# Kernel optimization log

Measured on AMD Instinct MI355X. Metric: run time of the kernel, lower is better.

Reference implementation:

```python
import jax, jax.numpy as jnp
import numpy as np

H = 64
N_BENE, N_DIAG, N_TREAT = 200000, 10000, 100000
E = 1000000
N_INST = 500000

def setup_inputs() -> dict:
    key = jax.random.key(0)
    ks = jax.random.split(key, 24)
    def lin(k, din, dout):
        kw, kb = jax.random.split(k)
        s = 1.0 / np.sqrt(din)
        return (jax.random.uniform(kw, (din, dout), jnp.float32, -s, s),
                jax.random.uniform(kb, (dout,), jnp.float32, -s, s))
    inp = {
        'bene_ids': jax.random.randint(ks[0], (N_BENE,), 0, 10000, jnp.int32),
        'diag_ids': jax.random.randint(ks[1], (N_DIAG,), 0, 200, jnp.int32),
        'treatment_ids': jax.random.randint(ks[2], (N_TREAT,), 0, 1000, jnp.int32),
        'b2d_src': jax.random.randint(ks[3], (E,), 0, N_BENE, jnp.int32),
        'b2d_dst': jax.random.randint(ks[4], (E,), 0, N_DIAG, jnp.int32),
        't2d_src': jax.random.randint(ks[5], (E,), 0, N_TREAT, jnp.int32),
        't2d_dst': jax.random.randint(ks[6], (E,), 0, N_DIAG, jnp.int32),
        'inst2type': jax.random.randint(ks[7], (N_INST,), 0, N_DIAG, jnp.int32),
        'bene_emb': jax.random.normal(ks[8], (10000, H), jnp.float32),
        'diag_emb': jax.random.normal(ks[9], (200, H), jnp.float32),
        'treat_emb': jax.random.normal(ks[10], (1000, H), jnp.float32),
    }
    # two conv layers: msg_bene_to_diag (Wb,bb), msg_treatment_to_diag (Wt,bt), update_diag (Wu,bu)
    names = ['Wb0','bb0','Wt0','bt0','Wu0','bu0','Wb1','bb1','Wt1','bt1','Wu1','bu1']
    idx = 11
    for i in range(0, len(names), 2):
        W, b = lin(ks[idx], H, H); idx += 1
        inp[names[i]] = W; inp[names[i+1]] = b
    inp['oW1'], inp['ob1'] = lin(ks[idx], H, H // 2); idx += 1
    inp['oW2'], inp['ob2'] = lin(ks[idx], H // 2, 1)
    return inp

def _conv(bene, diag, treat, b2d_src, b2d_dst, t2d_src, t2d_dst, Wb, bb, Wt, bt, Wu, bu):
    msg_b = bene[b2d_src] @ Wb + bb                      # [E, H]
    agg_b = jax.ops.segment_sum(msg_b, b2d_dst, num_segments=N_DIAG)
    msg_t = treat[t2d_src] @ Wt + bt                     # [E, H]
    agg_t = jax.ops.segment_sum(msg_t, t2d_dst, num_segments=N_DIAG)
    combined = 0.5 * (agg_b + agg_t)                     # mean over 2 message types
    return combined @ Wu + bu

def reference(bene_ids, diag_ids, treatment_ids, b2d_src, b2d_dst, t2d_src, t2d_dst,
              inst2type, bene_emb, diag_emb, treat_emb,
              Wb0, bb0, Wt0, bt0, Wu0, bu0, Wb1, bb1, Wt1, bt1, Wu1, bu1,
              oW1, ob1, oW2, ob2):
    bene = bene_emb[bene_ids]
    diag = diag_emb[diag_ids]
    treat = treat_emb[treatment_ids]
    for (Wb, bb, Wt, bt, Wu, bu) in ((Wb0, bb0, Wt0, bt0, Wu0, bu0),
                                     (Wb1, bb1, Wt1, bt1, Wu1, bu1)):
        diag = _conv(bene, diag, treat, b2d_src, b2d_dst, t2d_src, t2d_dst,
                     Wb, bb, Wt, bt, Wu, bu)
        bene, diag, treat = jax.nn.relu(bene), jax.nn.relu(diag), jax.nn.relu(treat)
    inst = diag[inst2type]                               # [N_INST, H]
    h = jax.nn.relu(inst @ oW1 + ob1)                    # dropout is eval-mode identity
    return jax.nn.sigmoid(h @ oW2 + ob2)[:, 0]
```

## Files before the change

kernel.cpp:

```cpp
#include <hip/hip_runtime.h>
#include <hip/hip_bf16.h>

#define Hdim 64
#define NDIAG 10000
#define NEDGE 1000000
#define NINST 500000

#define NSUP 79
#define SSHIFT 7
#define SMASK 127
#define CAP_S 13568
#define BUFK 96
#define EPB 3907
#define NSPLIT 4
#define FPSCALE 1048576.0f
#define FPINV (1.0f / 1048576.0f)

__global__ __launch_bounds__(512) void split_kernel(
    const int* __restrict__ b2d_dst, const int* __restrict__ b2d_src, const int* __restrict__ bene_ids,
    const int* __restrict__ t2d_dst, const int* __restrict__ t2d_src, const int* __restrict__ treat_ids,
    int* __restrict__ gcur_b, int* __restrict__ gbuf_b,
    int* __restrict__ gcur_t, int* __restrict__ gbuf_t) {
    const int ty = blockIdx.y;
    const int* dst  = ty ? t2d_dst  : b2d_dst;
    const int* src  = ty ? t2d_src  : b2d_src;
    const int* ids  = ty ? treat_ids: bene_ids;
    int* gcur = ty ? gcur_t : gcur_b;
    int* gbuf = ty ? gbuf_t : gbuf_b;

    __shared__ int buf[NSUP][BUFK];
    __shared__ int cnt[NSUP];
    __shared__ int base_s[NSUP];
    const int tid = threadIdx.x;
    for (int i = tid; i < NSUP; i += 512) cnt[i] = 0;
    __syncthreads();

    const int base = blockIdx.x * EPB;
    const int end = min(NEDGE, base + EPB);
    for (int e = base + tid; e < end; e += 512) {
        int d = dst[e];
        int c = ids[src[e]];
        int b = d >> SSHIFT;
        int v = ((d & SMASK) << 16) | c;
        int p = atomicAdd(&cnt[b], 1);
        if (p < BUFK) {
            buf[b][p] = v;
        } else {
            int gp = atomicAdd(&gcur[b], 1);
            if (gp < CAP_S) gbuf[b * CAP_S + gp] = v;
        }
    }
    __syncthreads();

    const int wid = tid >> 6, lane = tid & 63;
    if (wid < 2) {
        int b = (wid << 6) + lane;
        if (b < NSUP) {
            int n = min(cnt[b], BUFK);
            base_s[b] = atomicAdd(&gcur[b], n);
        }
    }
    __syncthreads();

    for (int b = wid; b < NSUP; b += 8) {
        int n = min(cnt[b], BUFK);
        int gp0 = base_s[b];
        for (int k = lane; k < n; k += 64) {
            int gp = gp0 + k;
            if (gp < CAP_S) gbuf[b * CAP_S + gp] = buf[b][k];
        }
    }
}

__global__ __launch_bounds__(512) void agg_kernel(
    const int* __restrict__ gbuf_b, const int* __restrict__ gcur_b, const float* __restrict__ bene_emb,
    const int* __restrict__ gbuf_t, const int* __restrict__ gcur_t, const float* __restrict__ treat_emb,
    int* __restrict__ pbuf, int* __restrict__ pbufd) {
    const int bk = blockIdx.x, ty = blockIdx.y, sp = blockIdx.z;
    const int* gbuf  = ty ? gbuf_t : gbuf_b;
    const int* gcur  = ty ? gcur_t : gcur_b;
    const float* emb = ty ? treat_emb : bene_emb;

    __shared__ int acc[128][64];
    __shared__ int dcw[8][2][64];

    const int tid = threadIdx.x;
    const int wid = tid >> 6, lane = tid & 63;
    int4* a4 = (int4*)&acc[0][0];
    for (int i = tid; i < 2048; i += 512) a4[i] = int4{0, 0, 0, 0};
    __syncthreads();

    const int count = min(gcur[bk], CAP_S);
    const int slice = (count + NSPLIT - 1) / NSPLIT;
    const int s0 = sp * slice;
    const int s1 = min(count, s0 + slice);
    const int n = max(0, s1 - s0);
    const int nfull = n >> 6;
    const int rem = n & 63;
    const int* bucket = gbuf + bk * CAP_S;

    int dc0 = 0, dc1 = 0;
    for (int ck = wid; ck < nfull; ck += 8) {
        int vv = bucket[s0 + (ck << 6) + lane];
        #pragma unroll
        for (int g = 0; g < 8; ++g) {
            int dl[8]; float vf[8];
            #pragma unroll
            for (int u = 0; u < 8; ++u) {
                int s = __builtin_amdgcn_readlane(vv, g * 8 + u);
                dl[u] = (s >> 16) & SMASK;
                vf[u] = emb[(s & 0xffff) * Hdim + lane];
            }
            #pragma unroll
            for (int u = 0; u < 8; ++u) {
                atomicAdd(&acc[dl[u]][lane], (int)(fmaxf(vf[u], 0.f) * FPSCALE));
                dc0 += ((dl[u] < 64) & (lane == (dl[u] & 63))) ? 1 : 0;
                dc1 += ((dl[u] >= 64) & (lane == (dl[u] & 63))) ? 1 : 0;
            }
        }
    }
    if (rem && wid == (nfull & 7)) {
        int base2 = s0 + (nfull << 6);
        int vv = (lane < rem) ? bucket[base2 + lane] : 0;
        for (int u = 0; u < rem; ++u) {
            int s = __builtin_amdgcn_readlane(vv, u);
            int dl = (s >> 16) & SMASK;
            float vf = emb[(s & 0xffff) * Hdim + lane];
            atomicAdd(&acc[dl][lane], (int)(fmaxf(vf, 0.f) * FPSCALE));
            dc0 += ((dl < 64) & (lane == (dl & 63))) ? 1 : 0;
            dc1 += ((dl >= 64) & (lane == (dl & 63))) ? 1 : 0;
        }
    }
    dcw[wid][0][lane] = dc0;
    dcw[wid][1][lane] = dc1;
    __syncthreads();

    int4* o4 = (int4*)(pbuf + (size_t)((ty * NSUP + bk) * NSPLIT + sp) * 8192);
    for (int i = tid; i < 2048; i += 512) o4[i] = a4[i];
    if (tid < 128) {
        int t = 0;
        #pragma unroll
        for (int w = 0; w < 8; ++w) t += dcw[w][tid >> 6][tid & 63];
        pbufd[(size_t)((ty * NSUP + bk) * NSPLIT + sp) * 128 + tid] = t;
    }
}

__global__ __launch_bounds__(256) void head_kernel(
    const int* __restrict__ pbuf, const int* __restrict__ pbufd,
    const float* __restrict__ Wb1, const float* __restrict__ bb1,
    const float* __restrict__ Wt1, const float* __restrict__ bt1,
    const float* __restrict__ Wu1, const float* __restrict__ bu1,
    const float* __restrict__ oW1, const float* __restrict__ ob1,
    const float* __restrict__ oW2, const float* __restrict__ ob2,
    float* __restrict__ per_diag_out) {
    int wave = threadIdx.x >> 6;
    int lane = threadIdx.x & 63;
    int d = blockIdx.x * 4 + wave;

    __shared__ float Sb[4][64];
    __shared__ float St[4][64];
    __shared__ float Cc[4][64];
    __shared__ float Dd[4][64];

    const int bk = d >> SSHIFT, row = d & SMASK;
    const int* pb = pbuf + (size_t)(bk * NSPLIT) * 8192;
    const int* pt = pbuf + (size_t)((NSUP + bk) * NSPLIT) * 8192;
    int sbi = 0, sti = 0, dgb = 0, dgt = 0;
    #pragma unroll
    for (int sp = 0; sp < NSPLIT; ++sp) {
        sbi += pb[sp * 8192 + row * 64 + lane];
        sti += pt[sp * 8192 + row * 64 + lane];
        dgb += pbufd[(size_t)(bk * NSPLIT + sp) * 128 + row];
        dgt += pbufd[(size_t)((NSUP + bk) * NSPLIT + sp) * 128 + row];
    }
    Sb[wave][lane] = (float)sbi * FPINV;
    St[wave][lane] = (float)sti * FPINV;
    __syncthreads();

    float ab = (float)dgb * bb1[lane];
    float at = (float)dgt * bt1[lane];
    #pragma unroll 8
    for (int l = 0; l < Hdim; ++l) {
        ab += Sb[wave][l] * Wb1[l * Hdim + lane];
        at += St[wave][l] * Wt1[l * Hdim + lane];
    }
    float comb = 0.5f * (ab + at);
    Cc[wave][lane] = comb;
    __syncthreads();

    float dg = bu1[lane];
    #pragma unroll 8
    for (int l = 0; l < Hdim; ++l) dg += Cc[wave][l] * Wu1[l * Hdim + lane];
    float d1 = fmaxf(dg, 0.f);
    Dd[wave][lane] = d1;
    __syncthreads();

    float contrib = 0.f;
    if (lane < 32) {
        float h = ob1[lane];
        #pragma unroll 8
        for (int l = 0; l < Hdim; ++l) h += Dd[wave][l] * oW1[l * 32 + lane];
        h = fmaxf(h, 0.f);
        contrib = h * oW2[lane];
    }
    for (int o = 32; o > 0; o >>= 1) contrib += __shfl_down(contrib, o);
    if (lane == 0) {
        float logit = contrib + ob2[0];
        per_diag_out[d] = 1.f / (1.f + __expf(-logit));
    }
}

__global__ void gather_kernel(const int* __restrict__ inst2type,
                              const float* __restrict__ per_diag_out,
                              float* __restrict__ out) {
    int i = blockIdx.x * blockDim.x + threadIdx.x;
    int i4 = i * 4;
    if (i4 >= NINST) return;
    int4 t = *reinterpret_cast<const int4*>(inst2type + i4);
    float4 r;
    r.x = per_diag_out[t.x];
    r.y = per_diag_out[t.y];
    r.z = per_diag_out[t.z];
    r.w = per_diag_out[t.w];
    *reinterpret_cast<float4*>(out + i4) = r;
}

extern "C" void kernel_launch(void* const* d_in, const int* in_sizes, int n_in,
                              void* d_out, int out_size, void* d_ws, size_t ws_size,
                              hipStream_t stream) {
    (void)in_sizes; (void)n_in; (void)out_size; (void)ws_size;

    const int*   bene_ids  = (const int*)d_in[0];
    const int*   treat_ids = (const int*)d_in[2];
    const int*   b2d_src   = (const int*)d_in[3];
    const int*   b2d_dst   = (const int*)d_in[4];
    const int*   t2d_src   = (const int*)d_in[5];
    const int*   t2d_dst   = (const int*)d_in[6];
    const int*   inst2type = (const int*)d_in[7];
    const float* bene_emb  = (const float*)d_in[8];
    const float* treat_emb = (const float*)d_in[10];
    const float* Wb1 = (const float*)d_in[17];
    const float* bb1 = (const float*)d_in[18];
    const float* Wt1 = (const float*)d_in[19];
    const float* bt1 = (const float*)d_in[20];
    const float* Wu1 = (const float*)d_in[21];
    const float* bu1 = (const float*)d_in[22];
    const float* oW1 = (const float*)d_in[23];
    const float* ob1 = (const float*)d_in[24];
    const float* oW2 = (const float*)d_in[25];
    const float* ob2 = (const float*)d_in[26];
    float* out = (float*)d_out;

    char* w = (char*)d_ws;
    auto alloc = [&](size_t bytes) {
        char* p = w;
        w += (bytes + 255) & ~(size_t)255;
        return p;
    };
    int* gcur_all = (int*)alloc(2 * NSUP * 4);
    int* gcur_b = gcur_all;
    int* gcur_t = gcur_all + NSUP;
    int* gbuf_b = (int*)alloc((size_t)NSUP * CAP_S * 4);
    int* gbuf_t = (int*)alloc((size_t)NSUP * CAP_S * 4);
    int* pbuf   = (int*)alloc((size_t)2 * NSUP * NSPLIT * 8192 * 4);
    int* pbufd  = (int*)alloc((size_t)2 * NSUP * NSPLIT * 128 * 4);
    float* pdo  = (float*)alloc(NDIAG * 4);

    hipMemsetAsync(gcur_all, 0, 2 * NSUP * 4, stream);

    split_kernel<<<dim3(256, 2), 512, 0, stream>>>(
        b2d_dst, b2d_src, bene_ids, t2d_dst, t2d_src, treat_ids,
        gcur_b, gbuf_b, gcur_t, gbuf_t);

    agg_kernel<<<dim3(NSUP, 2, NSPLIT), 512, 0, stream>>>(
        gbuf_b, gcur_b, bene_emb, gbuf_t, gcur_t, treat_emb, pbuf, pbufd);

    head_kernel<<<NDIAG / 4, 256, 0, stream>>>(
        pbuf, pbufd,
        Wb1, bb1, Wt1, bt1, Wu1, bu1, oW1, ob1, oW2, ob2, pdo);

    gather_kernel<<<(NINST / 4 + 255) / 256, 256, 0, stream>>>(inst2type, pdo, out);
}
```

Before: 233.1 us.

## Precompute fixed-point relu tables, vectorize split loads, simplify degree histogram

A new prep kernel converts the bene and treat embedding tables to relu'd fixed-point ints once and also zeroes the bucket counters, replacing the memset. The agg kernel then reads those ints directly, skipping per-edge relu and conversion, and computes per-diag degree counts with a shared-memory histogram in place of per-lane compare chains. The split kernel now loads four edges per thread with int4 loads, using smaller blocks and more of them. The cost is an extra kernel launch and a pass over the embedding tables, plus more shared-memory atomic traffic on the histogram.

```diff
diff --git a/kernel.cpp b/kernel.cpp
--- a/kernel.cpp
+++ b/kernel.cpp
@@ -5,16 +5,33 @@
 #define NDIAG 10000
 #define NEDGE 1000000
 #define NINST 500000
+#define NBENE_EMB 10000
+#define NTREAT_EMB 1000
 
 #define NSUP 79
 #define SSHIFT 7
 #define SMASK 127
 #define CAP_S 13568
-#define BUFK 96
-#define EPB 3907
+#define BUFK 64
+#define EPB 2048
+#define NSPB 489
 #define NSPLIT 4
 #define FPSCALE 1048576.0f
 #define FPINV (1.0f / 1048576.0f)
+
+__global__ __launch_bounds__(512) void prep_kernel(
+    const float* __restrict__ bene_emb, const float* __restrict__ treat_emb,
+    int* __restrict__ itab_b, int* __restrict__ itab_t, int* __restrict__ gcur_all) {
+    int gid = blockIdx.x * 512 + threadIdx.x;
+    if (gid < 2 * NSUP) gcur_all[gid] = 0;
+    if (gid < NBENE_EMB * Hdim) {
+        itab_b[gid] = (int)(fmaxf(bene_emb[gid], 0.f) * FPSCALE);
+    } else {
+        int g2 = gid - NBENE_EMB * Hdim;
+        if (g2 < NTREAT_EMB * Hdim)
+            itab_t[g2] = (int)(fmaxf(treat_emb[g2], 0.f) * FPSCALE);
+    }
+}
 
 __global__ __launch_bounds__(512) void split_kernel(
     const int* __restrict__ b2d_dst, const int* __restrict__ b2d_src, const int* __restrict__ bene_ids,
@@ -35,19 +52,26 @@
     for (int i = tid; i < NSUP; i += 512) cnt[i] = 0;
     __syncthreads();
 
-    const int base = blockIdx.x * EPB;
-    const int end = min(NEDGE, base + EPB);
-    for (int e = base + tid; e < end; e += 512) {
-        int d = dst[e];
-        int c = ids[src[e]];
-        int b = d >> SSHIFT;
-        int v = ((d & SMASK) << 16) | c;
-        int p = atomicAdd(&cnt[b], 1);
-        if (p < BUFK) {
-            buf[b][p] = v;
-        } else {
-            int gp = atomicAdd(&gcur[b], 1);
-            if (gp < CAP_S) gbuf[b * CAP_S + gp] = v;
+    const int e4 = blockIdx.x * EPB + tid * 4;
+    if (e4 < NEDGE) {
+        int4 d4 = *reinterpret_cast<const int4*>(dst + e4);
+        int4 s4 = *reinterpret_cast<const int4*>(src + e4);
+        int dd[4] = {d4.x, d4.y, d4.z, d4.w};
+        int ss[4] = {s4.x, s4.y, s4.z, s4.w};
+        int cc[4];
+        #pragma unroll
+        for (int u = 0; u < 4; ++u) cc[u] = ids[ss[u]];
+        #pragma unroll
+        for (int u = 0; u < 4; ++u) {
+            int b = dd[u] >> SSHIFT;
+            int v = ((dd[u] & SMASK) << 16) | cc[u];
+            int p = atomicAdd(&cnt[b], 1);
+            if (p < BUFK) {
+                buf[b][p] = v;
+            } else {
+                int gp = atomicAdd(&gcur[b], 1);
+                if (gp < CAP_S) gbuf[b * CAP_S + gp] = v;
+            }
         }
     }
     __syncthreads();
@@ -73,21 +97,22 @@
 }
 
 __global__ __launch_bounds__(512) void agg_kernel(
-    const int* __restrict__ gbuf_b, const int* __restrict__ gcur_b, const float* __restrict__ bene_emb,
-    const int* __restrict__ gbuf_t, const int* __restrict__ gcur_t, const float* __restrict__ treat_emb,
+    const int* __restrict__ gbuf_b, const int* __restrict__ gcur_b, const int* __restrict__ itab_b,
+    const int* __restrict__ gbuf_t, const int* __restrict__ gcur_t, const int* __restrict__ itab_t,
     int* __restrict__ pbuf, int* __restrict__ pbufd) {
     const int bk = blockIdx.x, ty = blockIdx.y, sp = blockIdx.z;
-    const int* gbuf  = ty ? gbuf_t : gbuf_b;
-    const int* gcur  = ty ? gcur_t : gcur_b;
-    const float* emb = ty ? treat_emb : bene_emb;
+    const int* gbuf = ty ? gbuf_t : gbuf_b;
+    const int* gcur = ty ? gcur_t : gcur_b;
+    const int* itab = ty ? itab_t : itab_b;
 
     __shared__ int acc[128][64];
-    __shared__ int dcw[8][2][64];
+    __shared__ int dhist[128];
 
     const int tid = threadIdx.x;
     const int wid = tid >> 6, lane = tid & 63;
     int4* a4 = (int4*)&acc[0][0];
     for (int i = tid; i < 2048; i += 512) a4[i] = int4{0, 0, 0, 0};
+    if (tid < 128) dhist[tid] = 0;
     __syncthreads();
 
     const int count = min(gcur[bk], CAP_S);
@@ -99,50 +124,38 @@
     const int rem = n & 63;
     const int* bucket = gbuf + bk * CAP_S;
 
-    int dc0 = 0, dc1 = 0;
     for (int ck = wid; ck < nfull; ck += 8) {
         int vv = bucket[s0 + (ck << 6) + lane];
+        atomicAdd(&dhist[(vv >> 16) & SMASK], 1);
         #pragma unroll
         for (int g = 0; g < 8; ++g) {
-            int dl[8]; float vf[8];
+            int dla[8], iv[8];
             #pragma unroll
             for (int u = 0; u < 8; ++u) {
                 int s = __builtin_amdgcn_readlane(vv, g * 8 + u);
-                dl[u] = (s >> 16) & SMASK;
-                vf[u] = emb[(s & 0xffff) * Hdim + lane];
+                dla[u] = (s >> 16) & SMASK;
+                iv[u] = itab[(s & 0xffff) * Hdim + lane];
             }
             #pragma unroll
-            for (int u = 0; u < 8; ++u) {
-                atomicAdd(&acc[dl[u]][lane], (int)(fmaxf(vf[u], 0.f) * FPSCALE));
-                dc0 += ((dl[u] < 64) & (lane == (dl[u] & 63))) ? 1 : 0;
-                dc1 += ((dl[u] >= 64) & (lane == (dl[u] & 63))) ? 1 : 0;
-            }
+            for (int u = 0; u < 8; ++u)
+                atomicAdd(&acc[dla[u]][lane], iv[u]);
         }
     }
     if (rem && wid == (nfull & 7)) {
         int base2 = s0 + (nfull << 6);
         int vv = (lane < rem) ? bucket[base2 + lane] : 0;
+        if (lane < rem) atomicAdd(&dhist[(vv >> 16) & SMASK], 1);
         for (int u = 0; u < rem; ++u) {
             int s = __builtin_amdgcn_readlane(vv, u);
-            int dl = (s >> 16) & SMASK;
-            float vf = emb[(s & 0xffff) * Hdim + lane];
-            atomicAdd(&acc[dl][lane], (int)(fmaxf(vf, 0.f) * FPSCALE));
-            dc0 += ((dl < 64) & (lane == (dl & 63))) ? 1 : 0;
-            dc1 += ((dl >= 64) & (lane == (dl & 63))) ? 1 : 0;
-        }
-    }
-    dcw[wid][0][lane] = dc0;
-    dcw[wid][1][lane] = dc1;
+            atomicAdd(&acc[(s >> 16) & SMASK][lane], itab[(s & 0xffff) * Hdim + lane]);
+        }
+    }
     __syncthreads();
 
     int4* o4 = (int4*)(pbuf + (size_t)((ty * NSUP + bk) * NSPLIT + sp) * 8192);
     for (int i = tid; i < 2048; i += 512) o4[i] = a4[i];
-    if (tid < 128) {
-        int t = 0;
-        #pragma unroll
-        for (int w = 0; w < 8; ++w) t += dcw[w][tid >> 6][tid & 63];
-        pbufd[(size_t)((ty * NSUP + bk) * NSPLIT + sp) * 128 + tid] = t;
-    }
+    if (tid < 128)
+        pbufd[(size_t)((ty * NSUP + bk) * NSPLIT + sp) * 128 + tid] = dhist[tid];
 }
 
 __global__ __launch_bounds__(256) void head_kernel(
@@ -262,18 +275,21 @@
     int* gcur_t = gcur_all + NSUP;
     int* gbuf_b = (int*)alloc((size_t)NSUP * CAP_S * 4);
     int* gbuf_t = (int*)alloc((size_t)NSUP * CAP_S * 4);
+    int* itab_b = (int*)alloc((size_t)NBENE_EMB * Hdim * 4);
+    int* itab_t = (int*)alloc((size_t)NTREAT_EMB * Hdim * 4);
     int* pbuf   = (int*)alloc((size_t)2 * NSUP * NSPLIT * 8192 * 4);
     int* pbufd  = (int*)alloc((size_t)2 * NSUP * NSPLIT * 128 * 4);
     float* pdo  = (float*)alloc(NDIAG * 4);
 
-    hipMemsetAsync(gcur_all, 0, 2 * NSUP * 4, stream);
-
-    split_kernel<<<dim3(256, 2), 512, 0, stream>>>(
+    prep_kernel<<<(NBENE_EMB + NTREAT_EMB) * Hdim / 512, 512, 0, stream>>>(
+        bene_emb, treat_emb, itab_b, itab_t, gcur_all);
+
+    split_kernel<<<dim3(NSPB, 2), 512, 0, stream>>>(
         b2d_dst, b2d_src, bene_ids, t2d_dst, t2d_src, treat_ids,
         gcur_b, gbuf_b, gcur_t, gbuf_t);
 
     agg_kernel<<<dim3(NSUP, 2, NSPLIT), 512, 0, stream>>>(
-        gbuf_b, gcur_b, bene_emb, gbuf_t, gcur_t, treat_emb, pbuf, pbufd);
+        gbuf_b, gcur_b, itab_b, gbuf_t, gcur_t, itab_t, pbuf, pbufd);
 
     head_kernel<<<NDIAG / 4, 256, 0, stream>>>(
         pbuf, pbufd,
```

Measured after the change: 213.1 us. 1.09x faster.
